# Performance work log

Hardware: AMD Instinct MI355X
Metric: run time of the kernel (lower is better)

Reference implementation:

```python
import jax, jax.numpy as jnp
import numpy as np

SIZE = 256
K = 100000.0
EPS = 1e-05


def setup_inputs() -> dict:
    key = jax.random.key(0)
    contour = jax.random.uniform(key, (4, 2, 64, 2), dtype=jnp.float32)  # values in [0,1)
    return {"contour": contour}


def reference(contour):
    b, n, kv, _ = contour.shape
    c = contour.reshape(b * n, 1, kv, 2)  # (bn, 1, k, 2)

    # mesh: torch.meshgrid default 'ij' indexing, stacked, flattened, normalized
    ii, jj = jnp.meshgrid(jnp.arange(SIZE), jnp.arange(SIZE), indexing="ij")
    mesh = jnp.stack([ii, jj], axis=-1).reshape(-1, 2).astype(contour.dtype) / SIZE
    mesh = mesh[None, :, None, :]  # (1, size^2, 1, 2)

    diff = c - mesh                              # (bn, size^2, k, 2)
    roll_diff = jnp.roll(diff, -1, axis=2)       # next vertex
    s = diff * jnp.roll(roll_diff, 1, axis=3)    # swap x/y of roll_diff (cross terms)
    sign = jnp.tanh(K * (s[..., 1] - s[..., 0])) # smooth sign of 2D cross product

    norm_diff = jnp.linalg.norm(diff, axis=3)
    norm_roll = jnp.linalg.norm(roll_diff, axis=3)
    scalar_product = jnp.sum(diff * roll_diff, axis=3)
    clip = jnp.clip(scalar_product / (norm_diff * norm_roll), -1.0 + EPS, 1.0 - EPS)
    angles = jnp.arccos(clip)                    # (bn, size^2, k)

    sum_angles = jnp.clip(jnp.abs(jnp.sum(sign * angles, axis=2) / (2.0 * jnp.pi)), 0.0, 1.0)
    return sum_angles.reshape(b, n, SIZE, SIZE)
```

## Files before the change

kernel.cpp:

```cpp
#include <hip/hip_runtime.h>
#include <math.h>

#define SIZE 256
#define KV 64
#define EPSC 1e-05f
#define STHR 6.0e-05f
#define SL_EPS 4e-09f

__device__ __forceinline__ float tanh_K(float s) {
    const float C = 288539.00817779f;
    float e = __builtin_amdgcn_exp2f(C * s);
    return fmaf(-2.0f, __builtin_amdgcn_rcpf(e + 1.0f), 1.0f);
}

__device__ __forceinline__ float fast_acos(float x) {
    float ax = fabsf(x);
    float p = fmaf(ax, -0.0187293f, 0.0742610f);
    p = fmaf(ax, p, -0.2121144f);
    p = fmaf(ax, p, 1.5707288f);
    float r = __builtin_amdgcn_sqrtf(1.0f - ax) * p;
    return (x >= 0.0f) ? r : ((float)M_PI - r);
}

__device__ __forceinline__ float corr_term(float2 c0, float2 c1,
                                           float mx, float my, float sgn) {
    float dx = c0.x - mx, dy = c0.y - my;
    float nx = c1.x - mx, ny = c1.y - my;
    float se = __fmul_rn(dy, nx) - __fmul_rn(dx, ny);
    float dot = fmaf(dx, nx, dy * ny);
    float n2 = fmaf(dx, dx, dy * dy) * fmaf(nx, nx, ny * ny);
    float r = dot * __builtin_amdgcn_rsqf(n2);
    r = fminf(fmaxf(r, -1.0f + EPSC), 1.0f - EPSC);
    return (tanh_K(se) - sgn) * fast_acos(r);
}

__global__ __launch_bounds__(256) void contour_to_mask_kernel(
    const float* __restrict__ contour,
    float* __restrict__ out)
{
    __shared__ float2 sc[KV];
    __shared__ float4 cons[KV];
    __shared__ __attribute__((aligned(16))) int   diffA[4][272];
    __shared__ __attribute__((aligned(16))) float corrA[4][256];
    __shared__ int wcnt[4];
    __shared__ int wlist[4][32];

    const int wave = threadIdx.x >> 6;
    const int lane = threadIdx.x & 63;
    const int img  = blockIdx.x >> 6;
    const int col  = ((blockIdx.x & 63) << 2) + wave;
    const float mx = (float)col * (1.0f / SIZE);

    const float* cbase = contour + img * 2 * KV;
    if (threadIdx.x < 2 * KV)
        ((float*)sc)[threadIdx.x] = cbase[threadIdx.x];
    __syncthreads();
    if (threadIdx.x < KV) {
        int k = threadIdx.x, k1 = (k + 1) & (KV - 1);
        float ckx = sc[k].x, cky = sc[k].y;
        float c1x = sc[k1].x, c1y = sc[k1].y;
        cons[k] = make_float4(cky * c1x - ckx * c1y, c1x - ckx, c1y - cky, 0.0f);
    }
    int*   diff = diffA[wave];
    float* corr = corrA[wave];
#pragma unroll
    for (int t = 0; t < 4; ++t) { diff[lane + 64 * t] = 0; corr[lane + 64 * t] = 0.0f; }
    if (lane == 0) { diff[256] = 0; wcnt[wave] = 0; }
    __syncthreads();

    {
        const int k = lane, k1 = (k + 1) & (KV - 1);
        const float4 cn = cons[k];
        const float A = cn.x, ey = cn.z;
        const float cky = sc[k].y, c1y = sc[k1].y;
        const float s0 = fmaf(mx, ey, A);
        const float sl = cn.y * (1.0f / SIZE);

        const int y0 = (int)ceilf((float)SIZE * cky);
        const int y1 = (int)ceilf((float)SIZE * c1y);

        int nlo, nhi;
        bool wide = false;
        int bl = 0, bh = 0;
        const float asl = fabsf(sl);
        if (asl >= SL_EPS) {
            const float jst = s0 / sl;
            const float jc = fminf(fmaxf(jst, -2.0e6f), 2.0e6f);
            if (sl > 0.0f) {
                nlo = max(0, min(SIZE, (int)floorf(jc) + 1)); nhi = SIZE;
            } else {
                nlo = 0; nhi = max(0, min(SIZE, (int)ceilf(jc)));
            }
            const float wband = STHR / asl;
            const float blo = jst - wband, bhi = jst + wband;
            if (bhi > -1.0f && blo < (float)SIZE) {
                if (wband > 6.0f) wide = true;
                else { bl = max(0, (int)floorf(blo));
                       bh = min(SIZE, (int)ceilf(bhi) + 1); }
            }
        } else {
            nlo = 0; nhi = (s0 < 0.0f) ? SIZE : 0;
            if (fabsf(s0) < STHR + 2.0e-6f) wide = true;
        }

        int ua = max(y0, nlo), ub = min(y1, nhi);
        if (ua < ub) { atomicAdd(&diff[ua], 1); atomicAdd(&diff[ub], -1); }
        int clo, chi;
        if (nlo == 0) { clo = nhi; chi = SIZE; } else { clo = 0; chi = nlo; }
        int da = max(y1, clo), db = min(y0, chi);
        if (da < db) { atomicAdd(&diff[da], -1); atomicAdd(&diff[db], 1); }

        if (wide) {
            int idx = atomicAdd(&wcnt[wave], 1);
            if (idx < 32) wlist[wave][idx] = k | (nlo << 6) | (nhi << 15);
        } else if (bl < bh) {
            const float2 c0 = sc[k], c1 = sc[k1];
            for (int j = bl; j < bh; ++j) {
                float sj = fmaf(-(float)j, sl, s0);
                if (fabsf(sj) < 4.0f * STHR) {
                    float my = (float)j * (1.0f / SIZE);
                    float sgn = (j >= nlo && j < nhi) ? -1.0f : 1.0f;
                    atomicAdd(&corr[j], corr_term(c0, c1, mx, my, sgn));
                }
            }
        }
    }
    __syncthreads();

    {
        const int nw = min(wcnt[wave], 32);
        for (int t = 0; t < nw; ++t) {
            const int e = wlist[wave][t];
            const int k = e & 63;
            const int nlo = (e >> 6) & 511, nhi = (e >> 15) & 511;
            const int k1 = (k + 1) & (KV - 1);
            const float4 cn = cons[k];
            const float s0 = fmaf(mx, cn.z, cn.x);
            const float sl = cn.y * (1.0f / SIZE);
            const float2 c0 = sc[k], c1 = sc[k1];
#pragma unroll
            for (int u = 0; u < 4; ++u) {
                const int j = 4 * lane + u;
                const float sj = fmaf(-(float)j, sl, s0);
                if (fabsf(sj) < STHR) {
                    const float my = (float)j * (1.0f / SIZE);
                    const float sgn = (j >= nlo && j < nhi) ? -1.0f : 1.0f;
                    corr[j] += corr_term(c0, c1, mx, my, sgn);
                }
            }
        }
    }
    __syncthreads();

    const int4   dq = ((const int4*)diff)[lane];
    const float4 cq = ((const float4*)corr)[lane];
    const int p0 = dq.x;
    const int p1 = p0 + dq.y;
    const int p2 = p1 + dq.z;
    const int p3 = p2 + dq.w;
    int scan = p3;
#pragma unroll
    for (int d = 1; d < 64; d <<= 1) {
        int up = __shfl_up(scan, d, 64);
        if (lane >= d) scan += up;
    }
    const int excl = scan - p3;

    const float TWO_PI = 6.283185307179586f;
    const float inv2pi = 0.15915494309189535f;
    float4 o;
    o.x = fminf(fabsf(fmaf(-TWO_PI, (float)(excl + p0), cq.x)) * inv2pi, 1.0f);
    o.y = fminf(fabsf(fmaf(-TWO_PI, (float)(excl + p1), cq.y)) * inv2pi, 1.0f);
    o.z = fminf(fabsf(fmaf(-TWO_PI, (float)(excl + p2), cq.z)) * inv2pi, 1.0f);
    o.w = fminf(fabsf(fmaf(-TWO_PI, (float)(excl + p3), cq.w)) * inv2pi, 1.0f);
    ((float4*)out)[img * 16384 + col * 64 + lane] = o;
}

extern "C" void kernel_launch(void* const* d_in, const int* in_sizes, int n_in,
                              void* d_out, int out_size, void* d_ws, size_t ws_size,
                              hipStream_t stream) {
    const float* contour = (const float*)d_in[0];
    float* out = (float*)d_out;
    contour_to_mask_kernel<<<512, 256, 0, stream>>>(contour, out);
}
```

Baseline: 55.61 us.

## Use one wave per block and ballot-driven wide-edge processing

The kernel moves from 4 waves per 256-thread block to single-wave 64-thread blocks, one output column each, launching 2048 blocks. The shared precomputed edge-constant table and the shared wide-edge list are dropped. Each lane now computes its edge constants in registers, and wide edges are walked with a ballot mask and shuffles. This removes block-level barriers and shared-memory bookkeeping, but adds more blocks and per-block contour loads. It also uses atomics on corr in the wide path, where the old code used plain adds.

Result: no change. 54.75 us (-1.6%).

```diff
diff --git a/kernel.cpp b/kernel.cpp
--- a/kernel.cpp
+++ b/kernel.cpp
@@ -34,119 +34,93 @@
     return (tanh_K(se) - sgn) * fast_acos(r);
 }
 
-__global__ __launch_bounds__(256) void contour_to_mask_kernel(
+__global__ __launch_bounds__(64) void contour_to_mask_kernel(
     const float* __restrict__ contour,
     float* __restrict__ out)
 {
     __shared__ float2 sc[KV];
-    __shared__ float4 cons[KV];
-    __shared__ __attribute__((aligned(16))) int   diffA[4][272];
-    __shared__ __attribute__((aligned(16))) float corrA[4][256];
-    __shared__ int wcnt[4];
-    __shared__ int wlist[4][32];
+    __shared__ __attribute__((aligned(16))) int   diff[272];
+    __shared__ __attribute__((aligned(16))) float corr[256];
 
-    const int wave = threadIdx.x >> 6;
-    const int lane = threadIdx.x & 63;
-    const int img  = blockIdx.x >> 6;
-    const int col  = ((blockIdx.x & 63) << 2) + wave;
+    const int lane = threadIdx.x;
+    const int img  = blockIdx.x >> 8;
+    const int col  = blockIdx.x & 255;
     const float mx = (float)col * (1.0f / SIZE);
 
-    const float* cbase = contour + img * 2 * KV;
-    if (threadIdx.x < 2 * KV)
-        ((float*)sc)[threadIdx.x] = cbase[threadIdx.x];
-    __syncthreads();
-    if (threadIdx.x < KV) {
-        int k = threadIdx.x, k1 = (k + 1) & (KV - 1);
-        float ckx = sc[k].x, cky = sc[k].y;
-        float c1x = sc[k1].x, c1y = sc[k1].y;
-        cons[k] = make_float4(cky * c1x - ckx * c1y, c1x - ckx, c1y - cky, 0.0f);
-    }
-    int*   diff = diffA[wave];
-    float* corr = corrA[wave];
+    sc[lane] = ((const float2*)(contour + img * 2 * KV))[lane];
 #pragma unroll
     for (int t = 0; t < 4; ++t) { diff[lane + 64 * t] = 0; corr[lane + 64 * t] = 0.0f; }
-    if (lane == 0) { diff[256] = 0; wcnt[wave] = 0; }
+    if (lane < 16) diff[256 + lane] = 0;
     __syncthreads();
 
+    const int k1 = (lane + 1) & (KV - 1);
+    const float2 c0 = sc[lane], c1 = sc[k1];
+    const float A  = c0.y * c1.x - c0.x * c1.y;
+    const float ex = c1.x - c0.x;
+    const float ey = c1.y - c0.y;
+    const float s0 = fmaf(mx, ey, A);
+    const float sl = ex * (1.0f / SIZE);
+
+    const int y0 = (int)ceilf((float)SIZE * c0.y);
+    const int y1 = (int)ceilf((float)SIZE * c1.y);
+
+    int nlo, nhi;
+    bool wide = false;
+    int bl = 0, bh = 0;
+    const float asl = fabsf(sl);
+    if (asl >= SL_EPS) {
+        const float jst = s0 / sl;
+        const float jc = fminf(fmaxf(jst, -2.0e6f), 2.0e6f);
+        if (sl > 0.0f) { nlo = max(0, min(SIZE, (int)floorf(jc) + 1)); nhi = SIZE; }
+        else           { nlo = 0; nhi = max(0, min(SIZE, (int)ceilf(jc))); }
+        const float wband = STHR / asl;
+        const float blo = jst - wband, bhi = jst + wband;
+        if (bhi > -1.0f && blo < (float)SIZE) {
+            if (wband > 6.0f) wide = true;
+            else { bl = max(0, (int)floorf(blo)); bh = min(SIZE, (int)ceilf(bhi) + 1); }
+        }
+    } else {
+        nlo = 0; nhi = (s0 < 0.0f) ? SIZE : 0;
+        if (fabsf(s0) < STHR + 2.0e-6f) wide = true;
+    }
+
     {
-        const int k = lane, k1 = (k + 1) & (KV - 1);
-        const float4 cn = cons[k];
-        const float A = cn.x, ey = cn.z;
-        const float cky = sc[k].y, c1y = sc[k1].y;
-        const float s0 = fmaf(mx, ey, A);
-        const float sl = cn.y * (1.0f / SIZE);
-
-        const int y0 = (int)ceilf((float)SIZE * cky);
-        const int y1 = (int)ceilf((float)SIZE * c1y);
-
-        int nlo, nhi;
-        bool wide = false;
-        int bl = 0, bh = 0;
-        const float asl = fabsf(sl);
-        if (asl >= SL_EPS) {
-            const float jst = s0 / sl;
-            const float jc = fminf(fmaxf(jst, -2.0e6f), 2.0e6f);
-            if (sl > 0.0f) {
-                nlo = max(0, min(SIZE, (int)floorf(jc) + 1)); nhi = SIZE;
-            } else {
-                nlo = 0; nhi = max(0, min(SIZE, (int)ceilf(jc)));
-            }
-            const float wband = STHR / asl;
-            const float blo = jst - wband, bhi = jst + wband;
-            if (bhi > -1.0f && blo < (float)SIZE) {
-                if (wband > 6.0f) wide = true;
-                else { bl = max(0, (int)floorf(blo));
-                       bh = min(SIZE, (int)ceilf(bhi) + 1); }
-            }
-        } else {
-            nlo = 0; nhi = (s0 < 0.0f) ? SIZE : 0;
-            if (fabsf(s0) < STHR + 2.0e-6f) wide = true;
-        }
-
         int ua = max(y0, nlo), ub = min(y1, nhi);
         if (ua < ub) { atomicAdd(&diff[ua], 1); atomicAdd(&diff[ub], -1); }
         int clo, chi;
         if (nlo == 0) { clo = nhi; chi = SIZE; } else { clo = 0; chi = nlo; }
         int da = max(y1, clo), db = min(y0, chi);
         if (da < db) { atomicAdd(&diff[da], -1); atomicAdd(&diff[db], 1); }
+    }
 
-        if (wide) {
-            int idx = atomicAdd(&wcnt[wave], 1);
-            if (idx < 32) wlist[wave][idx] = k | (nlo << 6) | (nhi << 15);
-        } else if (bl < bh) {
-            const float2 c0 = sc[k], c1 = sc[k1];
-            for (int j = bl; j < bh; ++j) {
-                float sj = fmaf(-(float)j, sl, s0);
-                if (fabsf(sj) < 4.0f * STHR) {
-                    float my = (float)j * (1.0f / SIZE);
-                    float sgn = (j >= nlo && j < nhi) ? -1.0f : 1.0f;
-                    atomicAdd(&corr[j], corr_term(c0, c1, mx, my, sgn));
-                }
+    if (!wide && bl < bh) {
+        for (int j = bl; j < bh; ++j) {
+            float sj = fmaf(-(float)j, sl, s0);
+            if (fabsf(sj) < 4.0f * STHR) {
+                float my = (float)j * (1.0f / SIZE);
+                float sgn = (j >= nlo && j < nhi) ? -1.0f : 1.0f;
+                atomicAdd(&corr[j], corr_term(c0, c1, mx, my, sgn));
             }
         }
     }
-    __syncthreads();
 
-    {
-        const int nw = min(wcnt[wave], 32);
-        for (int t = 0; t < nw; ++t) {
-            const int e = wlist[wave][t];
-            const int k = e & 63;
-            const int nlo = (e >> 6) & 511, nhi = (e >> 15) & 511;
-            const int k1 = (k + 1) & (KV - 1);
-            const float4 cn = cons[k];
-            const float s0 = fmaf(mx, cn.z, cn.x);
-            const float sl = cn.y * (1.0f / SIZE);
-            const float2 c0 = sc[k], c1 = sc[k1];
+    unsigned long long wmask = __ballot(wide);
+    while (wmask) {
+        const int k = __ffsll(wmask) - 1;
+        wmask &= wmask - 1;
+        const float s0k = __shfl(s0, k);
+        const float slk = __shfl(sl, k);
+        const int nlok = __shfl(nlo, k);
+        const int nhik = __shfl(nhi, k);
+        const float2 ck0 = sc[k], ck1 = sc[(k + 1) & (KV - 1)];
 #pragma unroll
-            for (int u = 0; u < 4; ++u) {
-                const int j = 4 * lane + u;
-                const float sj = fmaf(-(float)j, sl, s0);
-                if (fabsf(sj) < STHR) {
-                    const float my = (float)j * (1.0f / SIZE);
-                    const float sgn = (j >= nlo && j < nhi) ? -1.0f : 1.0f;
-                    corr[j] += corr_term(c0, c1, mx, my, sgn);
-                }
+        for (int u = 0; u < 4; ++u) {
+            const int j = 4 * lane + u;
+            const float sj = fmaf(-(float)j, slk, s0k);
+            if (fabsf(sj) < STHR) {
+                const float my = (float)j * (1.0f / SIZE);
+                const float sgn = (j >= nlok && j < nhik) ? -1.0f : 1.0f;
+                atomicAdd(&corr[j], corr_term(ck0, ck1, mx, my, sgn));
             }
         }
     }
@@ -181,5 +155,5 @@
                               hipStream_t stream) {
     const float* contour = (const float*)d_in[0];
     float* out = (float*)d_out;
-    contour_to_mask_kernel<<<512, 256, 0, stream>>>(contour, out);
+    contour_to_mask_kernel<<<2048, 64, 0, stream>>>(contour, out);
 }
```
